# Kernel tuning notes

Hardware: AMD Instinct MI355X
Metric: run time of the kernel (lower is better)

The kernel has to match this reference:

```python
import jax, jax.numpy as jnp
import numpy as np

B, L, D, H, NC = 32, 1024, 256, 512, 16


def setup_inputs() -> dict:
    key = jax.random.key(0)
    ks = jax.random.split(key, 8)
    s_in = 1.0 / np.sqrt(D)
    s_h = 1.0 / np.sqrt(H)
    return {
        "x": jax.random.normal(ks[0], (B, L, D), jnp.float32),
        "W0": jax.random.normal(ks[1], (D, 4 * H), jnp.float32) * s_in,
        "b0": jnp.zeros((2 * H,), jnp.float32),
        "W1": jax.random.normal(ks[2], (H, 3 * H), jnp.float32) * s_h,
        "b1": jnp.zeros((2 * H,), jnp.float32),
        "W2": jax.random.normal(ks[3], (H, 3 * H), jnp.float32) * s_h,
        "b2": jnp.zeros((2 * H,), jnp.float32),
        "W3": jax.random.normal(ks[4], (H, 3 * H), jnp.float32) * s_h,
        "b3": jnp.zeros((2 * H,), jnp.float32),
        "Wp": jax.random.normal(ks[5], (H, H), jnp.float32) * s_h,
        "bp": jnp.zeros((H,), jnp.float32),
        "Wc": jax.random.normal(ks[6], (H, NC), jnp.float32) * s_h,
        "bc": jnp.zeros((NC,), jnp.float32),
    }


def _sru_layer(h, W, b, first):
    # h: (B, L, Din); W: (Din, kH); b: (2H,)
    k = 4 if first else 3
    Hh = W.shape[1] // k
    U = jnp.einsum('bld,dk->blk', h, W)  # (B, L, kH)
    if first:
        xt, fpre, rpre, xres = jnp.split(U, 4, axis=-1)
    else:
        xt, fpre, rpre = jnp.split(U, 3, axis=-1)
        xres = h
    bf, br = jnp.split(b, 2)
    f = jax.nn.sigmoid(fpre + bf)  # forget gate (B, L, H)
    r = jax.nn.sigmoid(rpre + br)  # reset/highway gate

    def step(c, inp):
        f_t, x_t = inp
        c = f_t * c + (1.0 - f_t) * x_t
        return c, c

    c0 = jnp.zeros((h.shape[0], Hh), h.dtype)
    _, c_seq = jax.lax.scan(step, c0, (jnp.swapaxes(f, 0, 1), jnp.swapaxes(xt, 0, 1)))
    c_seq = jnp.swapaxes(c_seq, 0, 1)  # (B, L, H)
    out = r * c_seq + (1.0 - r) * xres  # highway output
    return out, c_seq[:, -1, :]


def reference(x, W0, b0, W1, b1, W2, b2, W3, b3, Wp, bp, Wc, bc):
    h = x
    finals = []
    for W, b, first in ((W0, b0, True), (W1, b1, False), (W2, b2, False), (W3, b3, False)):
        h, cT = _sru_layer(h, W, b, first)
        finals.append(cT)
    hidden = jnp.stack(finals)  # (num_layers, B, H)
    projected = h[:, -1, :] @ Wp + bp
    output = projected @ Wc + bc
    return output, h, hidden
```

## Files before the change

### kernel.cpp

```cpp
#include <hip/hip_runtime.h>

#define DEV_INLINE __device__ __forceinline__

typedef __attribute__((ext_vector_type(8))) short bf16x8;
typedef __attribute__((ext_vector_type(4))) float f32x4;

DEV_INLINE unsigned short f2bf(float f) {
  union { float f; unsigned u; } v; v.f = f;
  unsigned r = v.u + 0x7FFFu + ((v.u >> 16) & 1u);
  return (unsigned short)(r >> 16);
}
DEV_INLINE float bf2f(unsigned short u) {
  union { unsigned u; float f; } v; v.u = ((unsigned)u) << 16;
  return v.f;
}
DEV_INLINE float sigmoidf_(float x) { return 1.0f / (1.0f + __expf(-x)); }

DEV_INLINE void gload_lds16(const void* g, void* l) {
  __builtin_amdgcn_global_load_lds(
      (const __attribute__((address_space(1))) void*)(g),
      (__attribute__((address_space(3))) void*)(l), 16, 0, 0);
}

__global__ __launch_bounds__(256)
void prep_kernel(const float* __restrict__ x, unsigned short* __restrict__ xbf,
                 const float* __restrict__ W0, unsigned short* __restrict__ Wt0,
                 const float* __restrict__ W1, unsigned short* __restrict__ Wt1,
                 const float* __restrict__ W2, unsigned short* __restrict__ Wt2,
                 const float* __restrict__ W3, unsigned short* __restrict__ Wt3) {
  __shared__ float tile[32][33];
  const int id = blockIdx.x;
  const int t = threadIdx.x;
  if (id < 8192) {
    const int i = id * 256 + t;
    const float4 v = reinterpret_cast<const float4*>(x)[i];
    ushort4 o;
    o.x = f2bf(v.x); o.y = f2bf(v.y); o.z = f2bf(v.z); o.w = f2bf(v.w);
    reinterpret_cast<ushort4*>(xbf)[i] = o;
    return;
  }
  int rid = id - 8192;
  const float* W; unsigned short* Wt; int K, N, bx, by;
  if (rid < 512) {
    W = W0; Wt = Wt0; K = 256; N = 2048; bx = rid & 7; by = rid >> 3;
  } else {
    rid -= 512;
    const int seg = rid / 768; rid -= seg * 768;
    K = 512; N = 1536;
    W  = seg == 0 ? W1  : (seg == 1 ? W2  : W3);
    Wt = seg == 0 ? Wt1 : (seg == 1 ? Wt2 : Wt3);
    bx = rid & 15; by = rid >> 4;
  }
  const int tx = t & 31, ty = t >> 5;
  const int kb = bx * 32, nb = by * 32;
  #pragma unroll
  for (int i = 0; i < 32; i += 8)
    tile[ty + i][tx] = W[(size_t)(kb + ty + i) * N + (nb + tx)];
  __syncthreads();
  #pragma unroll
  for (int i = 0; i < 32; i += 8)
    Wt[(size_t)(nb + ty + i) * K + (kb + tx)] = f2bf(tile[tx][ty + i]);
}

__global__ __launch_bounds__(256, 4)
void gemm_gate_kernel(const unsigned short* __restrict__ A,
                      const unsigned short* __restrict__ Bt,
                      const float* __restrict__ bias,
                      unsigned short* __restrict__ U,
                      int N, int K, int NTN) {
  __shared__ short smem[2 * 128 * 64];
  short* As = smem;
  short* Bs = smem + 128 * 64;

  const int tid = threadIdx.x;
  const int lane = tid & 63;
  const int l15 = lane & 15;
  const int l4 = lane >> 4;
  const int w = tid >> 6;
  const int wr = (w >> 1) * 64;
  const int wc = (w & 1) * 64;

  const int nwg = gridDim.x;
  const int cpx = nwg >> 3;
  const int swz = (blockIdx.x & 7) * cpx + (blockIdx.x >> 3);
  const int mtile = swz / NTN;
  const int ntile = swz - mtile * NTN;
  const int m0 = mtile * 128;
  const int n0 = ntile * 128;

  f32x4 acc[4][4];
  #pragma unroll
  for (int i = 0; i < 4; ++i)
    #pragma unroll
    for (int j = 0; j < 4; ++j)
      acc[i][j] = (f32x4){0.f, 0.f, 0.f, 0.f};

  const unsigned short* Abase = A + (size_t)m0 * K;
  const unsigned short* Bbase = Bt + (size_t)n0 * K;
  const int nsteps = K >> 6;

  for (int t = 0; t < nsteps; ++t) {
    const int k0 = t * 64;
    #pragma unroll
    for (int it = 0; it < 4; ++it) {
      int c = it * 256 + tid;
      int row = c >> 3, sl = c & 7;
      int ks = sl ^ (row & 7);
      gload_lds16(Abase + (size_t)row * K + (k0 + ks * 8), &As[c * 8]);
    }
    #pragma unroll
    for (int it = 0; it < 4; ++it) {
      int c = it * 256 + tid;
      int row = c >> 3, sl = c & 7;
      int ks = sl ^ (row & 7);
      gload_lds16(Bbase + (size_t)row * K + (k0 + ks * 8), &Bs[c * 8]);
    }
    __syncthreads();

    const bf16x8* As8 = (const bf16x8*)As;
    const bf16x8* Bs8 = (const bf16x8*)Bs;
    #pragma unroll
    for (int kk = 0; kk < 2; ++kk) {
      bf16x8 af[4], bfr[4];
      #pragma unroll
      for (int i = 0; i < 4; ++i) {
        int r = wr + i * 16 + l15;
        int phys = (kk * 4 + l4) ^ (r & 7);
        af[i] = As8[r * 8 + phys];
      }
      #pragma unroll
      for (int j = 0; j < 4; ++j) {
        int r = wc + j * 16 + l15;
        int phys = (kk * 4 + l4) ^ (r & 7);
        bfr[j] = Bs8[r * 8 + phys];
      }
      #pragma unroll
      for (int i = 0; i < 4; ++i)
        #pragma unroll
        for (int j = 0; j < 4; ++j)
          acc[i][j] = __builtin_amdgcn_mfma_f32_16x16x32_bf16(af[i], bfr[j], acc[i][j], 0, 0, 0);
    }
    __syncthreads();
  }

  short* eps = smem;
  const int EL = 144;
  #pragma unroll
  for (int p = 0; p < 2; ++p) {
    __syncthreads();
    #pragma unroll
    for (int ii = 0; ii < 2; ++ii) {
      const int i = 2 * p + ii;
      #pragma unroll
      for (int j = 0; j < 4; ++j) {
        const int cg = n0 + wc + j * 16 + l15;
        const int region = cg >> 9;
        #pragma unroll
        for (int reg = 0; reg < 4; ++reg) {
          float v = acc[i][j][reg];
          if (region == 1)      v = sigmoidf_(v + bias[cg & 511]);
          else if (region == 2) v = sigmoidf_(v + bias[512 + (cg & 511)]);
          const int lr = (wr >> 1) + ii * 16 + l4 * 4 + reg;
          const int col = (wc + j * 16 + l15) ^ (((lr >> 2) & 3) << 3);
          eps[lr * EL + col] = (short)f2bf(v);
        }
      }
    }
    __syncthreads();
    const int lr2 = tid >> 2;
    const int grow = m0 + ((lr2 >> 5) << 6) + (2 * p + ((lr2 >> 4) & 1)) * 16 + (lr2 & 15);
    const int xorv = ((lr2 >> 2) & 3) << 3;
    unsigned short* urow = U + (size_t)grow * N + n0;
    #pragma unroll
    for (int k = 0; k < 4; ++k) {
      const int col = (tid & 3) * 8 + k * 32;
      bf16x8 vv = *(const bf16x8*)&eps[lr2 * EL + (col ^ xorv)];
      *(bf16x8*)(urow + col) = vv;
    }
  }
}

__global__ __launch_bounds__(512)
void scan_kernel(const unsigned short* __restrict__ U, int N, int first,
                 const unsigned short* __restrict__ hin,
                 unsigned short* __restrict__ hout_bf,
                 float* __restrict__ hout_f32,
                 float* __restrict__ hidden) {
  const int b = blockIdx.x >> 3;
  const int hslice = blockIdx.x & 7;
  const int hv = threadIdx.x & 7;
  const int ch = threadIdx.x >> 3;
  const int h0 = (hslice << 6) + (hv << 3);
  __shared__ float sP[64 * 68];
  __shared__ float sQ[64 * 68];

  const size_t rowBase = (size_t)b * 1024 + (size_t)ch * 16;
  const unsigned short* Uxt = U + rowBase * N + h0;

  float c[8], P[8];
  #pragma unroll
  for (int j = 0; j < 8; ++j) { c[j] = 0.f; P[j] = 1.f; }
  {
    const unsigned short* px = Uxt;
    const unsigned short* pf = Uxt + 512;
    #pragma unroll 2
    for (int l = 0; l < 16; ++l) {
      bf16x8 xv = *(const bf16x8*)px;
      bf16x8 fv = *(const bf16x8*)pf;
      #pragma unroll
      for (int j = 0; j < 8; ++j) {
        float f  = bf2f((unsigned short)fv[j]);
        float xt = bf2f((unsigned short)xv[j]);
        c[j] = f * c[j] + (1.f - f) * xt;
        P[j] *= f;
      }
      px += N; pf += N;
    }
  }
  float* myP = &sP[ch * 68 + hv * 8];
  float* myQ = &sQ[ch * 68 + hv * 8];
  #pragma unroll
  for (int j = 0; j < 8; ++j) { myP[j] = P[j]; myQ[j] = c[j]; }
  __syncthreads();

  for (int s = 1; s < 64; s <<= 1) {
    const int src = (ch >= s) ? (ch - s) : ch;
    float pp[8], pq[8];
    const float* qP = &sP[src * 68 + hv * 8];
    const float* qQ = &sQ[src * 68 + hv * 8];
    #pragma unroll
    for (int j = 0; j < 8; ++j) { pp[j] = qP[j]; pq[j] = qQ[j]; }
    asm volatile("s_waitcnt lgkmcnt(0)" ::: "memory");
    __builtin_amdgcn_sched_barrier(0);
    __syncthreads();
    if (ch >= s) {
      #pragma unroll
      for (int j = 0; j < 8; ++j) {
        c[j] = P[j] * pq[j] + c[j];
        P[j] = P[j] * pp[j];
        myP[j] = P[j]; myQ[j] = c[j];
      }
    }
    __syncthreads();
  }

  float cc[8];
  if (ch == 0) {
    #pragma unroll
    for (int j = 0; j < 8; ++j) cc[j] = 0.f;
  } else {
    const float* qQ = &sQ[(ch - 1) * 68 + hv * 8];
    #pragma unroll
    for (int j = 0; j < 8; ++j) cc[j] = qQ[j];
  }

  const unsigned short* px = Uxt;
  const unsigned short* pf = Uxt + 512;
  const unsigned short* pr = Uxt + 1024;
  const unsigned short* pxr = first ? (Uxt + 1536) : (hin + rowBase * 512 + h0);
  const int xr_stride = first ? N : 512;
  unsigned short* ob = hout_bf ? hout_bf + rowBase * 512 + h0 : (unsigned short*)nullptr;
  float* of = hout_f32 ? hout_f32 + rowBase * 512 + h0 : (float*)nullptr;
  #pragma unroll 2
  for (int l = 0; l < 16; ++l) {
    bf16x8 xv = *(const bf16x8*)px;
    bf16x8 fv = *(const bf16x8*)pf;
    bf16x8 rv = *(const bf16x8*)pr;
    bf16x8 xrv = *(const bf16x8*)pxr;
    bf16x8 obuf;
    float ofl[8];
    #pragma unroll
    for (int j = 0; j < 8; ++j) {
      float f  = bf2f((unsigned short)fv[j]);
      float xt = bf2f((unsigned short)xv[j]);
      cc[j] = f * cc[j] + (1.f - f) * xt;
      float r  = bf2f((unsigned short)rv[j]);
      float xr = bf2f((unsigned short)xrv[j]);
      float o = r * cc[j] + (1.f - r) * xr;
      obuf[j] = (short)f2bf(o);
      ofl[j] = o;
    }
    if (ob) { *(bf16x8*)ob = obuf; ob += 512; }
    if (of) {
      *(float4*)of = make_float4(ofl[0], ofl[1], ofl[2], ofl[3]);
      *(float4*)(of + 4) = make_float4(ofl[4], ofl[5], ofl[6], ofl[7]);
      of += 512;
    }
    px += N; pf += N; pr += N; pxr += xr_stride;
  }
  if (ch == 63) {
    #pragma unroll
    for (int j = 0; j < 8; ++j) hidden[(size_t)b * 512 + h0 + j] = cc[j];
  }
}

__global__ __launch_bounds__(256)
void proj_kernel(const float* __restrict__ hfull, const float* __restrict__ Wp,
                 const float* __restrict__ bp, const float* __restrict__ Wc,
                 const float* __restrict__ bc, float* __restrict__ out) {
  __shared__ float hl[512];
  __shared__ float pr[512];
  const int b = blockIdx.x, t = threadIdx.x;
  const float* hrow = hfull + ((size_t)b * 1024 + 1023) * 512;
  hl[t] = hrow[t];
  hl[t + 256] = hrow[t + 256];
  __syncthreads();
  for (int j = t; j < 512; j += 256) {
    float s = 0.f;
    for (int k = 0; k < 512; ++k) s += hl[k] * Wp[(size_t)k * 512 + j];
    pr[j] = s + bp[j];
  }
  __syncthreads();
  if (t < 16) {
    float s = 0.f;
    for (int k = 0; k < 512; ++k) s += pr[k] * Wc[k * 16 + t];
    out[b * 16 + t] = s + bc[t];
  }
}

extern "C" void kernel_launch(void* const* d_in, const int* in_sizes, int n_in,
                              void* d_out, int out_size, void* d_ws, size_t ws_size,
                              hipStream_t stream) {
  const float* x  = (const float*)d_in[0];
  const float* W0 = (const float*)d_in[1];
  const float* b0 = (const float*)d_in[2];
  const float* W1 = (const float*)d_in[3];
  const float* b1 = (const float*)d_in[4];
  const float* W2 = (const float*)d_in[5];
  const float* b2 = (const float*)d_in[6];
  const float* W3 = (const float*)d_in[7];
  const float* b3 = (const float*)d_in[8];
  const float* Wp = (const float*)d_in[9];
  const float* bp = (const float*)d_in[10];
  const float* Wc = (const float*)d_in[11];
  const float* bc = (const float*)d_in[12];

  float* out = (float*)d_out;
  float* outO = out;
  float* outH = out + 512;
  float* outHid = out + 512 + (size_t)32 * 1024 * 512;

  char* ws = (char*)d_ws;
  size_t off = 0;
  auto alloc = [&](size_t bytes) {
    void* p = ws + off;
    off += (bytes + 255) & ~(size_t)255;
    return p;
  };
  unsigned short* Wt0 = (unsigned short*)alloc((size_t)2048 * 256 * 2);
  unsigned short* Wt1 = (unsigned short*)alloc((size_t)1536 * 512 * 2);
  unsigned short* Wt2 = (unsigned short*)alloc((size_t)1536 * 512 * 2);
  unsigned short* Wt3 = (unsigned short*)alloc((size_t)1536 * 512 * 2);
  unsigned short* xbf = (unsigned short*)alloc((size_t)32768 * 256 * 2);
  unsigned short* h0  = (unsigned short*)alloc((size_t)32768 * 512 * 2);
  unsigned short* h1  = (unsigned short*)alloc((size_t)32768 * 512 * 2);
  unsigned short* Ubf = (unsigned short*)alloc((size_t)32768 * 2048 * 2);
  (void)ws_size; (void)in_sizes; (void)n_in; (void)out_size;

  prep_kernel<<<8192 + 512 + 3 * 768, 256, 0, stream>>>(
      x, xbf, W0, Wt0, W1, Wt1, W2, Wt2, W3, Wt3);

  gemm_gate_kernel<<<256 * 16, 256, 0, stream>>>(xbf, Wt0, b0, Ubf, 2048, 256, 16);
  scan_kernel<<<256, 512, 0, stream>>>(Ubf, 2048, 1, nullptr, h0, nullptr, outHid + 0);
  gemm_gate_kernel<<<256 * 12, 256, 0, stream>>>(h0, Wt1, b1, Ubf, 1536, 512, 12);
  scan_kernel<<<256, 512, 0, stream>>>(Ubf, 1536, 0, h0, h1, nullptr, outHid + 16384);
  gemm_gate_kernel<<<256 * 12, 256, 0, stream>>>(h1, Wt2, b2, Ubf, 1536, 512, 12);
  scan_kernel<<<256, 512, 0, stream>>>(Ubf, 1536, 0, h1, h0, nullptr, outHid + 32768);
  gemm_gate_kernel<<<256 * 12, 256, 0, stream>>>(h0, Wt3, b3, Ubf, 1536, 512, 12);
  scan_kernel<<<256, 512, 0, stream>>>(Ubf, 1536, 0, h0, nullptr, outH, outHid + 49152);

  proj_kernel<<<32, 256, 0, stream>>>(outH, Wp, bp, Wc, bc, outO);
}
```

Measured before the change: 559.1 us.

## Enlarge GEMM tile to 256x128 and write gate outputs directly

```diff
diff --git a/kernel.cpp b/kernel.cpp
--- a/kernel.cpp
+++ b/kernel.cpp
@@ -62,35 +62,35 @@
     Wt[(size_t)(nb + ty + i) * K + (kb + tx)] = f2bf(tile[tx][ty + i]);
 }
 
-__global__ __launch_bounds__(256, 4)
+__global__ __launch_bounds__(256, 2)
 void gemm_gate_kernel(const unsigned short* __restrict__ A,
                       const unsigned short* __restrict__ Bt,
                       const float* __restrict__ bias,
                       unsigned short* __restrict__ U,
                       int N, int K, int NTN) {
-  __shared__ short smem[2 * 128 * 64];
+  __shared__ short smem[256 * 64 + 128 * 64];
   short* As = smem;
-  short* Bs = smem + 128 * 64;
+  short* Bs = smem + 256 * 64;
 
   const int tid = threadIdx.x;
   const int lane = tid & 63;
   const int l15 = lane & 15;
   const int l4 = lane >> 4;
   const int w = tid >> 6;
-  const int wr = (w >> 1) * 64;
-  const int wc = (w & 1) * 64;
+  const int wrow = (w >> 1) * 128;
+  const int wcol = (w & 1) * 64;
 
   const int nwg = gridDim.x;
   const int cpx = nwg >> 3;
   const int swz = (blockIdx.x & 7) * cpx + (blockIdx.x >> 3);
   const int mtile = swz / NTN;
   const int ntile = swz - mtile * NTN;
-  const int m0 = mtile * 128;
+  const int m0 = mtile * 256;
   const int n0 = ntile * 128;
 
-  f32x4 acc[4][4];
-  #pragma unroll
-  for (int i = 0; i < 4; ++i)
+  f32x4 acc[8][4];
+  #pragma unroll
+  for (int i = 0; i < 8; ++i)
     #pragma unroll
     for (int j = 0; j < 4; ++j)
       acc[i][j] = (f32x4){0.f, 0.f, 0.f, 0.f};
@@ -102,7 +102,7 @@
   for (int t = 0; t < nsteps; ++t) {
     const int k0 = t * 64;
     #pragma unroll
-    for (int it = 0; it < 4; ++it) {
+    for (int it = 0; it < 8; ++it) {
       int c = it * 256 + tid;
       int row = c >> 3, sl = c & 7;
       int ks = sl ^ (row & 7);
@@ -121,21 +121,21 @@
     const bf16x8* Bs8 = (const bf16x8*)Bs;
     #pragma unroll
     for (int kk = 0; kk < 2; ++kk) {
-      bf16x8 af[4], bfr[4];
-      #pragma unroll
-      for (int i = 0; i < 4; ++i) {
-        int r = wr + i * 16 + l15;
+      bf16x8 af[8], bfr[4];
+      #pragma unroll
+      for (int i = 0; i < 8; ++i) {
+        int r = wrow + i * 16 + l15;
         int phys = (kk * 4 + l4) ^ (r & 7);
         af[i] = As8[r * 8 + phys];
       }
       #pragma unroll
       for (int j = 0; j < 4; ++j) {
-        int r = wc + j * 16 + l15;
+        int r = wcol + j * 16 + l15;
         int phys = (kk * 4 + l4) ^ (r & 7);
         bfr[j] = Bs8[r * 8 + phys];
       }
       #pragma unroll
-      for (int i = 0; i < 4; ++i)
+      for (int i = 0; i < 8; ++i)
         #pragma unroll
         for (int j = 0; j < 4; ++j)
           acc[i][j] = __builtin_amdgcn_mfma_f32_16x16x32_bf16(af[i], bfr[j], acc[i][j], 0, 0, 0);
@@ -143,39 +143,22 @@
     __syncthreads();
   }
 
-  short* eps = smem;
-  const int EL = 144;
-  #pragma unroll
-  for (int p = 0; p < 2; ++p) {
-    __syncthreads();
-    #pragma unroll
-    for (int ii = 0; ii < 2; ++ii) {
-      const int i = 2 * p + ii;
-      #pragma unroll
-      for (int j = 0; j < 4; ++j) {
-        const int cg = n0 + wc + j * 16 + l15;
-        const int region = cg >> 9;
-        #pragma unroll
-        for (int reg = 0; reg < 4; ++reg) {
-          float v = acc[i][j][reg];
-          if (region == 1)      v = sigmoidf_(v + bias[cg & 511]);
-          else if (region == 2) v = sigmoidf_(v + bias[512 + (cg & 511)]);
-          const int lr = (wr >> 1) + ii * 16 + l4 * 4 + reg;
-          const int col = (wc + j * 16 + l15) ^ (((lr >> 2) & 3) << 3);
-          eps[lr * EL + col] = (short)f2bf(v);
-        }
-      }
-    }
-    __syncthreads();
-    const int lr2 = tid >> 2;
-    const int grow = m0 + ((lr2 >> 5) << 6) + (2 * p + ((lr2 >> 4) & 1)) * 16 + (lr2 & 15);
-    const int xorv = ((lr2 >> 2) & 3) << 3;
-    unsigned short* urow = U + (size_t)grow * N + n0;
-    #pragma unroll
-    for (int k = 0; k < 4; ++k) {
-      const int col = (tid & 3) * 8 + k * 32;
-      bf16x8 vv = *(const bf16x8*)&eps[lr2 * EL + (col ^ xorv)];
-      *(bf16x8*)(urow + col) = vv;
+  #pragma unroll
+  for (int i = 0; i < 8; ++i) {
+    const int grow0 = m0 + wrow + i * 16 + l4 * 4;
+    #pragma unroll
+    for (int j = 0; j < 4; ++j) {
+      const int gcol = n0 + wcol + j * 16 + l15;
+      const int region = gcol >> 9;
+      const bool gate = (region == 1) | (region == 2);
+      const float bval = (region == 1) ? bias[gcol & 511]
+                       : ((region == 2) ? bias[512 + (gcol & 511)] : 0.f);
+      #pragma unroll
+      for (int reg = 0; reg < 4; ++reg) {
+        float v = acc[i][j][reg];
+        if (gate) v = sigmoidf_(v + bval);
+        U[(size_t)(grow0 + reg) * N + gcol] = f2bf(v);
+      }
     }
   }
 }
@@ -360,13 +343,13 @@
   prep_kernel<<<8192 + 512 + 3 * 768, 256, 0, stream>>>(
       x, xbf, W0, Wt0, W1, Wt1, W2, Wt2, W3, Wt3);
 
-  gemm_gate_kernel<<<256 * 16, 256, 0, stream>>>(xbf, Wt0, b0, Ubf, 2048, 256, 16);
+  gemm_gate_kernel<<<128 * 16, 256, 0, stream>>>(xbf, Wt0, b0, Ubf, 2048, 256, 16);
   scan_kernel<<<256, 512, 0, stream>>>(Ubf, 2048, 1, nullptr, h0, nullptr, outHid + 0);
-  gemm_gate_kernel<<<256 * 12, 256, 0, stream>>>(h0, Wt1, b1, Ubf, 1536, 512, 12);
+  gemm_gate_kernel<<<128 * 12, 256, 0, stream>>>(h0, Wt1, b1, Ubf, 1536, 512, 12);
   scan_kernel<<<256, 512, 0, stream>>>(Ubf, 1536, 0, h0, h1, nullptr, outHid + 16384);
-  gemm_gate_kernel<<<256 * 12, 256, 0, stream>>>(h1, Wt2, b2, Ubf, 1536, 512, 12);
+  gemm_gate_kernel<<<128 * 12, 256, 0, stream>>>(h1, Wt2, b2, Ubf, 1536, 512, 12);
   scan_kernel<<<256, 512, 0, stream>>>(Ubf, 1536, 0, h1, h0, nullptr, outHid + 32768);
-  gemm_gate_kernel<<<256 * 12, 256, 0, stream>>>(h0, Wt3, b3, Ubf, 1536, 512, 12);
+  gemm_gate_kernel<<<128 * 12, 256, 0, stream>>>(h0, Wt3, b3, Ubf, 1536, 512, 12);
   scan_kernel<<<256, 512, 0, stream>>>(Ubf, 1536, 0, h0, nullptr, outH, outHid + 49152);
 
   proj_kernel<<<32, 256, 0, stream>>>(outH, Wp, bp, Wc, bc, outO);
```

Result: no change. 569.5 us (+1.9%).

## Double-buffer LDS tiles in gate GEMM to overlap global loads with MFMA

Applied to the files above, without the earlier changes.

```diff
diff --git a/kernel.cpp b/kernel.cpp
--- a/kernel.cpp
+++ b/kernel.cpp
@@ -62,15 +62,13 @@
     Wt[(size_t)(nb + ty + i) * K + (kb + tx)] = f2bf(tile[tx][ty + i]);
 }
 
-__global__ __launch_bounds__(256, 4)
+__global__ __launch_bounds__(256, 2)
 void gemm_gate_kernel(const unsigned short* __restrict__ A,
                       const unsigned short* __restrict__ Bt,
                       const float* __restrict__ bias,
                       unsigned short* __restrict__ U,
                       int N, int K, int NTN) {
-  __shared__ short smem[2 * 128 * 64];
-  short* As = smem;
-  short* Bs = smem + 128 * 64;
+  __shared__ short smem[2 * 16384];
 
   const int tid = threadIdx.x;
   const int lane = tid & 63;
@@ -97,28 +95,44 @@
 
   const unsigned short* Abase = A + (size_t)m0 * K;
   const unsigned short* Bbase = Bt + (size_t)n0 * K;
-  const int nsteps = K >> 6;
-
-  for (int t = 0; t < nsteps; ++t) {
+  const int NT = K >> 6;
+
+  auto stage = [&](int t, int b) {
+    short* dA = smem + b * 16384;
+    short* dB = dA + 8192;
     const int k0 = t * 64;
     #pragma unroll
     for (int it = 0; it < 4; ++it) {
       int c = it * 256 + tid;
       int row = c >> 3, sl = c & 7;
       int ks = sl ^ (row & 7);
-      gload_lds16(Abase + (size_t)row * K + (k0 + ks * 8), &As[c * 8]);
+      gload_lds16(Abase + (size_t)row * K + (k0 + ks * 8), &dA[c * 8]);
     }
     #pragma unroll
     for (int it = 0; it < 4; ++it) {
       int c = it * 256 + tid;
       int row = c >> 3, sl = c & 7;
       int ks = sl ^ (row & 7);
-      gload_lds16(Bbase + (size_t)row * K + (k0 + ks * 8), &Bs[c * 8]);
-    }
-    __syncthreads();
-
-    const bf16x8* As8 = (const bf16x8*)As;
-    const bf16x8* Bs8 = (const bf16x8*)Bs;
+      gload_lds16(Bbase + (size_t)row * K + (k0 + ks * 8), &dB[c * 8]);
+    }
+  };
+
+  stage(0, 0);
+
+  for (int t = 0; t < NT; ++t) {
+    if (t + 1 < NT) {
+      stage(t + 1, (t + 1) & 1);
+      asm volatile("s_waitcnt vmcnt(8)" ::: "memory");
+    } else {
+      asm volatile("s_waitcnt vmcnt(0)" ::: "memory");
+    }
+    __builtin_amdgcn_sched_barrier(0);
+    asm volatile("s_barrier" ::: "memory");
+    __builtin_amdgcn_sched_barrier(0);
+
+    const short* bufc = smem + (t & 1) * 16384;
+    const bf16x8* As8 = (const bf16x8*)bufc;
+    const bf16x8* Bs8 = (const bf16x8*)(bufc + 8192);
     #pragma unroll
     for (int kk = 0; kk < 2; ++kk) {
       bf16x8 af[4], bfr[4];
@@ -140,7 +154,10 @@
         for (int j = 0; j < 4; ++j)
           acc[i][j] = __builtin_amdgcn_mfma_f32_16x16x32_bf16(af[i], bfr[j], acc[i][j], 0, 0, 0);
     }
-    __syncthreads();
+    asm volatile("s_waitcnt lgkmcnt(0)" ::: "memory");
+    __builtin_amdgcn_sched_barrier(0);
+    asm volatile("s_barrier" ::: "memory");
+    __builtin_amdgcn_sched_barrier(0);
   }
 
   short* eps = smem;
```

After: 649.0 us. 16.1% more time.

## Fuse fp32 input conversion into first GEMM and halve scan block size

Applied to the files above, without the earlier changes.

```diff
diff --git a/kernel.cpp b/kernel.cpp
--- a/kernel.cpp
+++ b/kernel.cpp
@@ -23,23 +23,13 @@
 }
 
 __global__ __launch_bounds__(256)
-void prep_kernel(const float* __restrict__ x, unsigned short* __restrict__ xbf,
-                 const float* __restrict__ W0, unsigned short* __restrict__ Wt0,
+void prep_kernel(const float* __restrict__ W0, unsigned short* __restrict__ Wt0,
                  const float* __restrict__ W1, unsigned short* __restrict__ Wt1,
                  const float* __restrict__ W2, unsigned short* __restrict__ Wt2,
                  const float* __restrict__ W3, unsigned short* __restrict__ Wt3) {
   __shared__ float tile[32][33];
-  const int id = blockIdx.x;
+  int rid = blockIdx.x;
   const int t = threadIdx.x;
-  if (id < 8192) {
-    const int i = id * 256 + t;
-    const float4 v = reinterpret_cast<const float4*>(x)[i];
-    ushort4 o;
-    o.x = f2bf(v.x); o.y = f2bf(v.y); o.z = f2bf(v.z); o.w = f2bf(v.w);
-    reinterpret_cast<ushort4*>(xbf)[i] = o;
-    return;
-  }
-  int rid = id - 8192;
   const float* W; unsigned short* Wt; int K, N, bx, by;
   if (rid < 512) {
     W = W0; Wt = Wt0; K = 256; N = 2048; bx = rid & 7; by = rid >> 3;
@@ -62,8 +52,9 @@
     Wt[(size_t)(nb + ty + i) * K + (kb + tx)] = f2bf(tile[tx][ty + i]);
 }
 
-__global__ __launch_bounds__(256, 4)
-void gemm_gate_kernel(const unsigned short* __restrict__ A,
+template <bool AF32>
+__global__ __launch_bounds__(256, 2)
+void gemm_gate_kernel(const void* __restrict__ Aptr,
                       const unsigned short* __restrict__ Bt,
                       const float* __restrict__ bias,
                       unsigned short* __restrict__ U,
@@ -95,18 +86,37 @@
     for (int j = 0; j < 4; ++j)
       acc[i][j] = (f32x4){0.f, 0.f, 0.f, 0.f};
 
-  const unsigned short* Abase = A + (size_t)m0 * K;
+  const unsigned short* Abf = (const unsigned short*)Aptr;
+  const float* Af = (const float*)Aptr;
   const unsigned short* Bbase = Bt + (size_t)n0 * K;
   const int nsteps = K >> 6;
 
   for (int t = 0; t < nsteps; ++t) {
     const int k0 = t * 64;
-    #pragma unroll
-    for (int it = 0; it < 4; ++it) {
-      int c = it * 256 + tid;
-      int row = c >> 3, sl = c & 7;
-      int ks = sl ^ (row & 7);
-      gload_lds16(Abase + (size_t)row * K + (k0 + ks * 8), &As[c * 8]);
+    if constexpr (AF32) {
+      #pragma unroll
+      for (int it = 0; it < 4; ++it) {
+        int c = it * 256 + tid;
+        int row = c >> 3, sl = c & 7;
+        int ks = sl ^ (row & 7);
+        const float* src = Af + (size_t)(m0 + row) * K + (k0 + ks * 8);
+        const float4 v0 = *(const float4*)src;
+        const float4 v1 = *(const float4*)(src + 4);
+        bf16x8 o;
+        o[0] = (short)f2bf(v0.x); o[1] = (short)f2bf(v0.y);
+        o[2] = (short)f2bf(v0.z); o[3] = (short)f2bf(v0.w);
+        o[4] = (short)f2bf(v1.x); o[5] = (short)f2bf(v1.y);
+        o[6] = (short)f2bf(v1.z); o[7] = (short)f2bf(v1.w);
+        *(bf16x8*)&As[c * 8] = o;
+      }
+    } else {
+      #pragma unroll
+      for (int it = 0; it < 4; ++it) {
+        int c = it * 256 + tid;
+        int row = c >> 3, sl = c & 7;
+        int ks = sl ^ (row & 7);
+        gload_lds16(Abf + (size_t)(m0 + row) * K + (k0 + ks * 8), &As[c * 8]);
+      }
     }
     #pragma unroll
     for (int it = 0; it < 4; ++it) {
@@ -180,19 +190,19 @@
   }
 }
 
-__global__ __launch_bounds__(512)
+__global__ __launch_bounds__(256)
 void scan_kernel(const unsigned short* __restrict__ U, int N, int first,
                  const unsigned short* __restrict__ hin,
                  unsigned short* __restrict__ hout_bf,
                  float* __restrict__ hout_f32,
                  float* __restrict__ hidden) {
-  const int b = blockIdx.x >> 3;
-  const int hslice = blockIdx.x & 7;
-  const int hv = threadIdx.x & 7;
-  const int ch = threadIdx.x >> 3;
-  const int h0 = (hslice << 6) + (hv << 3);
-  __shared__ float sP[64 * 68];
-  __shared__ float sQ[64 * 68];
+  const int b = blockIdx.x >> 4;
+  const int hslice = blockIdx.x & 15;
+  const int hv = threadIdx.x & 3;
+  const int ch = threadIdx.x >> 2;
+  const int h0 = (hslice << 5) + (hv << 3);
+  __shared__ float sP[64 * 36];
+  __shared__ float sQ[64 * 36];
 
   const size_t rowBase = (size_t)b * 1024 + (size_t)ch * 16;
   const unsigned short* Uxt = U + rowBase * N + h0;
@@ -217,8 +227,8 @@
       px += N; pf += N;
     }
   }
-  float* myP = &sP[ch * 68 + hv * 8];
-  float* myQ = &sQ[ch * 68 + hv * 8];
+  float* myP = &sP[ch * 36 + hv * 8];
+  float* myQ = &sQ[ch * 36 + hv * 8];
   #pragma unroll
   for (int j = 0; j < 8; ++j) { myP[j] = P[j]; myQ[j] = c[j]; }
   __syncthreads();
@@ -226,8 +236,8 @@
   for (int s = 1; s < 64; s <<= 1) {
     const int src = (ch >= s) ? (ch - s) : ch;
     float pp[8], pq[8];
-    const float* qP = &sP[src * 68 + hv * 8];
-    const float* qQ = &sQ[src * 68 + hv * 8];
+    const float* qP = &sP[src * 36 + hv * 8];
+    const float* qQ = &sQ[src * 36 + hv * 8];
     #pragma unroll
     for (int j = 0; j < 8; ++j) { pp[j] = qP[j]; pq[j] = qQ[j]; }
     asm volatile("s_waitcnt lgkmcnt(0)" ::: "memory");
@@ -249,7 +259,7 @@
     #pragma unroll
     for (int j = 0; j < 8; ++j) cc[j] = 0.f;
   } else {
-    const float* qQ = &sQ[(ch - 1) * 68 + hv * 8];
+    const float* qQ = &sQ[(ch - 1) * 36 + hv * 8];
     #pragma unroll
     for (int j = 0; j < 8; ++j) cc[j] = qQ[j];
   }
@@ -351,23 +361,21 @@
   unsigned short* Wt1 = (unsigned short*)alloc((size_t)1536 * 512 * 2);
   unsigned short* Wt2 = (unsigned short*)alloc((size_t)1536 * 512 * 2);
   unsigned short* Wt3 = (unsigned short*)alloc((size_t)1536 * 512 * 2);
-  unsigned short* xbf = (unsigned short*)alloc((size_t)32768 * 256 * 2);
   unsigned short* h0  = (unsigned short*)alloc((size_t)32768 * 512 * 2);
   unsigned short* h1  = (unsigned short*)alloc((size_t)32768 * 512 * 2);
   unsigned short* Ubf = (unsigned short*)alloc((size_t)32768 * 2048 * 2);
   (void)ws_size; (void)in_sizes; (void)n_in; (void)out_size;
 
-  prep_kernel<<<8192 + 512 + 3 * 768, 256, 0, stream>>>(
-      x, xbf, W0, Wt0, W1, Wt1, W2, Wt2, W3, Wt3);
-
-  gemm_gate_kernel<<<256 * 16, 256, 0, stream>>>(xbf, Wt0, b0, Ubf, 2048, 256, 16);
-  scan_kernel<<<256, 512, 0, stream>>>(Ubf, 2048, 1, nullptr, h0, nullptr, outHid + 0);
-  gemm_gate_kernel<<<256 * 12, 256, 0, stream>>>(h0, Wt1, b1, Ubf, 1536, 512, 12);
-  scan_kernel<<<256, 512, 0, stream>>>(Ubf, 1536, 0, h0, h1, nullptr, outHid + 16384);
-  gemm_gate_kernel<<<256 * 12, 256, 0, stream>>>(h1, Wt2, b2, Ubf, 1536, 512, 12);
-  scan_kernel<<<256, 512, 0, stream>>>(Ubf, 1536, 0, h1, h0, nullptr, outHid + 32768);
-  gemm_gate_kernel<<<256 * 12, 256, 0, stream>>>(h0, Wt3, b3, Ubf, 1536, 512, 12);
-  scan_kernel<<<256, 512, 0, stream>>>(Ubf, 1536, 0, h0, nullptr, outH, outHid + 49152);
+  prep_kernel<<<512 + 3 * 768, 256, 0, stream>>>(W0, Wt0, W1, Wt1, W2, Wt2, W3, Wt3);
+
+  gemm_gate_kernel<true><<<256 * 16, 256, 0, stream>>>(x, Wt0, b0, Ubf, 2048, 256, 16);
+  scan_kernel<<<512, 256, 0, stream>>>(Ubf, 2048, 1, nullptr, h0, nullptr, outHid + 0);
+  gemm_gate_kernel<false><<<256 * 12, 256, 0, stream>>>(h0, Wt1, b1, Ubf, 1536, 512, 12);
+  scan_kernel<<<512, 256, 0, stream>>>(Ubf, 1536, 0, h0, h1, nullptr, outHid + 16384);
+  gemm_gate_kernel<false><<<256 * 12, 256, 0, stream>>>(h1, Wt2, b2, Ubf, 1536, 512, 12);
+  scan_kernel<<<512, 256, 0, stream>>>(Ubf, 1536, 0, h1, h0, nullptr, outHid + 32768);
+  gemm_gate_kernel<false><<<256 * 12, 256, 0, stream>>>(h0, Wt3, b3, Ubf, 1536, 512, 12);
+  scan_kernel<<<512, 256, 0, stream>>>(Ubf, 1536, 0, h0, nullptr, outH, outHid + 49152);
 
   proj_kernel<<<32, 256, 0, stream>>>(outH, Wp, bp, Wc, bc, outO);
 }
```

Result: slower. 687.3 us (+22.9%).
